# Kernel optimization log

Measured on AMD Instinct MI355X. Metric: run time of the kernel, lower is better.

## Reference

```python
import jax, jax.numpy as jnp
import numpy as np

T, NC, NQ = 16, 32, 32
H, W, C = 128, 128, 1
DW, DR, DZ = 256, 256, 128
LABEL_DIM, Y_DIM = 2, 2
NHEADS = 8
NFEAT = int(DW * np.log(DW))  # performer default nb_features = int(d*ln d) = 1419


def setup_inputs() -> dict:
    key = jax.random.key(0)
    ks = iter(jax.random.split(key, 48))
    def nrm(shape, scale=0.02):
        return jax.random.normal(next(ks), shape, dtype=jnp.float32) * scale
    z = lambda *s: jnp.zeros(s, jnp.float32)
    return {
        'batch_train_images': jax.random.normal(next(ks), (T, NC, C, H, W), jnp.float32),
        'label_train': jax.random.normal(next(ks), (T, NC, LABEL_DIM), jnp.float32),
        'batch_test_images': jax.random.normal(next(ks), (T, NQ, C, H, W), jnp.float32),
        'conv1_w': nrm((32, C, 3, 3), 0.1), 'conv1_b': z(32),
        'conv2_w': nrm((48, 32, 3, 3), 0.05), 'conv2_b': z(48),
        'conv3_w': nrm((64, 48, 3, 3), 0.05), 'conv3_b': z(64),
        'enc_lw': nrm((DW, 4096)), 'enc_lb': z(DW),
        'ty_w': nrm((DW // 4, LABEL_DIM)), 'ty_b': z(DW // 4),
        'er_w1': nrm((DR, DW + DW // 4), 0.05), 'er_b1': z(DR),
        'er_w2': nrm((DR, DR), 0.05), 'er_b2': z(DR),
        'er_w3': nrm((DR, DR), 0.05), 'er_b3': z(DR),
        'wq': nrm((NHEADS, DW, DW), 0.05), 'wq_b': z(NHEADS, DW),
        'wk': nrm((NHEADS, DW, DW), 0.05), 'wk_b': z(NHEADS, DW),
        'wv': nrm((NHEADS, DW, DW), 0.05), 'wv_b': z(NHEADS, DW),
        'wo_w': nrm((DW, NHEADS * DW), 0.02), 'wo_b': z(DW),
        'rz_w': nrm((DZ, DR), 0.05), 'rz_b': z(DZ),
        'd0_w1': nrm((100, DW + DZ), 0.05), 'd0_b1': z(100),
        'd0_w2': nrm((100, 100), 0.05), 'd0_b2': z(100),
        'd0_w3': nrm((Y_DIM, 100), 0.05), 'd0_b3': z(Y_DIM),
        'proj': jax.random.normal(next(ks), (NFEAT, DW), jnp.float32),
    }


def _conv(x, w, b, stride):
    y = jax.lax.conv_general_dilated(x, w, (stride, stride), [(1, 1), (1, 1)],
                                     dimension_numbers=('NCHW', 'OIHW', 'NCHW'))
    return y + b[None, :, None, None]


def _maxpool2(x):
    return jax.lax.reduce_window(x, -jnp.inf, jax.lax.max, (1, 1, 2, 2), (1, 1, 2, 2), 'VALID')


def _encode(x, c1w, c1b, c2w, c2b, c3w, c3b, lw, lb):
    # BBBEncoder (mean weights): 128->64->32->pool16->8, 64ch, flatten 4096 -> DW
    x = jax.nn.relu(_conv(x, c1w, c1b, 2))
    x = jax.nn.relu(_conv(x, c2w, c2b, 2))
    x = _maxpool2(x)
    x = jax.nn.relu(_conv(x, c3w, c3b, 2))
    x = x.reshape(x.shape[0], -1)  # [B, 4096], NCHW order matches torch view
    return x @ lw.T + lb


def _softmax_kernel(x, proj, is_query):
    # performer softmax-kernel random features
    dn = x.shape[-1] ** -0.25
    ratio = proj.shape[0] ** -0.5
    xn = x * dn
    xd = jnp.einsum('bhnd,fd->bhnf', xn, proj)
    diag = 0.5 * jnp.sum(xn * xn, axis=-1, keepdims=True)
    if is_query:
        m = jnp.max(xd, axis=-1, keepdims=True)
    else:
        m = jnp.max(xd, axis=(-1, -2), keepdims=True)
    return ratio * (jnp.exp(xd - diag - jax.lax.stop_gradient(m)) + 1e-4)


def _forward(batch_train_images, label_train, batch_test_images,
             conv1_w, conv1_b, conv2_w, conv2_b, conv3_w, conv3_b, enc_lw, enc_lb,
             ty_w, ty_b, er_w1, er_b1, er_w2, er_b2, er_w3, er_b3,
             wq, wq_b, wk, wk_b, wv, wv_b, wo_w, wo_b, rz_w, rz_b,
             d0_w1, d0_b1, d0_w2, d0_b2, d0_w3, d0_b3, proj):
    enc = lambda im: _encode(im, conv1_w, conv1_b, conv2_w, conv2_b, conv3_w, conv3_b, enc_lw, enc_lb)
    x_qry = enc(batch_test_images.reshape(-1, C, H, W)).reshape(T, NQ, DW)
    x_ctx = enc(batch_train_images.reshape(-1, C, H, W)).reshape(T, NC, DW)
    ly = label_train @ ty_w.T + ty_b
    x = jnp.concatenate([x_ctx, ly], axis=2)  # [T, NC, DW + DW//4]
    h = jax.nn.relu(x @ er_w1.T + er_b1)
    h = jax.nn.relu(h @ er_w2.T + er_b2)
    rs = h @ er_w3.T + er_b3  # [T, NC, DR]
    # per-head projections (batched over the 8 heads)
    k_all = jnp.einsum('bnd,hed->bhne', x_ctx, wk) + wk_b[None, :, None, :]
    v_all = jnp.einsum('bnd,hed->bhne', rs, wv) + wv_b[None, :, None, :]
    q_all = jnp.einsum('bnd,hed->bhne', x_qry, wq) + wq_b[None, :, None, :]
    qp = _softmax_kernel(q_all, proj, True)   # [T, H, NQ, F]
    kp = _softmax_kernel(k_all, proj, False)  # [T, H, NC, F]
    d_inv = 1.0 / jnp.einsum('bhnf,bhf->bhn', qp, kp.sum(axis=2))
    ctx_mat = jnp.einsum('bhnf,bhne->bhfe', kp, v_all)
    outs = jnp.einsum('bhnf,bhfe->bhne', qp, ctx_mat) * d_inv[..., None]
    outs = outs.transpose(0, 2, 3, 1).reshape(T, NQ, -1)  # permute(0,2,3,1).view
    rep = outs @ wo_w.T + wo_b
    zz = rep @ rz_w.T + rz_b  # [T, NQ, DZ]
    xz = jnp.concatenate([x_qry, zz], axis=-1)
    h = jax.nn.relu(xz @ d0_w1.T + d0_b1)
    h = jax.nn.relu(h @ d0_w2.T + d0_b2)
    return jnp.tanh(h @ d0_w3.T + d0_b3)  # pr_y_mu [T, NQ, Y_DIM]


def reference(batch_train_images, label_train, batch_test_images,
              conv1_w, conv1_b, conv2_w, conv2_b, conv3_w, conv3_b, enc_lw, enc_lb,
              ty_w, ty_b, er_w1, er_b1, er_w2, er_b2, er_w3, er_b3,
              wq, wq_b, wk, wk_b, wv, wv_b, wo_w, wo_b, rz_w, rz_b,
              d0_w1, d0_b1, d0_w2, d0_b2, d0_w3, d0_b3, proj):
    pr_y_mu = _forward(batch_train_images, label_train, batch_test_images,
                       conv1_w, conv1_b, conv2_w, conv2_b, conv3_w, conv3_b, enc_lw, enc_lb,
                       ty_w, ty_b, er_w1, er_b1, er_w2, er_b2, er_w3, er_b3,
                       wq, wq_b, wk, wk_b, wv, wv_b, wo_w, wo_b, rz_w, rz_b,
                       d0_w1, d0_b1, d0_w2, d0_b2, d0_w3, d0_b3, proj)
    kl = jnp.float32(0.0)  # deterministic (mean-weight) BBB encoder -> KL constant
    return (pr_y_mu, kl)
```

## Files before the change

kernel.cpp:

```cpp
#include <hip/hip_runtime.h>
#include <math.h>

#define F_FEAT 1419
static constexpr float DN    = 0.25f;

typedef short short8 __attribute__((ext_vector_type(8)));
typedef float f32x4  __attribute__((ext_vector_type(4)));

static constexpr long OFF_XDQ  = 0;
static constexpr long OFF_XDK  = 5812224;
static constexpr long U_WQH = 0;
static constexpr long U_WQL = 524288;
static constexpr long U_WKH = 1048576;
static constexpr long U_WKL = 1572864;
static constexpr long U_WVH = 2097152;
static constexpr long U_WVL = 2621440;
static constexpr long OFF_ENCT = 4000000;
static constexpr long OFF_REPT = 6200000;
static constexpr long OFF_PA   = 11624448;
static constexpr long U_PH  = 23248896;
static constexpr long U_PL  = 23625728;
static constexpr long U_XCH = 24002560;
static constexpr long U_XCL = 24264704;
static constexpr long U_RSH = 24526848;
static constexpr long U_RSL = 24657920;
static constexpr long U_C3H = 25165824;
static constexpr long U_C3L = 29360128;
static constexpr long U_WOH = 25165824;
static constexpr long U_WOL = 25690112;
static constexpr long BASE     = 16777216;
static constexpr long OFF_XCTX = BASE + 0;
static constexpr long OFF_XQRY = BASE + 131072;
static constexpr long OFF_XCAT = BASE + 262144;
static constexpr long OFF_H1   = BASE + 425984;
static constexpr long OFF_H2   = BASE + 557056;
static constexpr long OFF_RS   = BASE + 688128;
static constexpr long U_QH  = (BASE + 819200) * 2;
static constexpr long U_QL  = U_QH + 1048576;
static constexpr long U_KH  = (BASE + 1867776) * 2;
static constexpr long U_KL  = U_KH + 1048576;
static constexpr long OFF_VA   = BASE + 2916352;
static constexpr long OFF_AW1  = BASE + 3964928;
static constexpr long U_ELH = (BASE + 3977344) * 2;
static constexpr long U_ELL = U_ELH + 1048576;
static constexpr long U_REPH = U_ELH;
static constexpr long U_REPL = U_ELL;
static constexpr long OFF_REP  = BASE + 5025920;
static constexpr long OFF_XZ   = BASE + 5156992;
static constexpr long OFF_DH1  = BASE + 5353600;
static constexpr long OFF_DH2  = BASE + 5404800;
static constexpr long OFF_MD   = BASE + 5456000;
static constexpr long OFF_AW   = 22233216;
static constexpr long OFF_AW3  = 22240128;

__device__ inline unsigned short f2bf(float f) {
    unsigned int x = __float_as_uint(f);
    unsigned int r = x + 0x7fffu + ((x >> 16) & 1u);
    return (unsigned short)(r >> 16);
}
__device__ inline float bf2f(unsigned short h) {
    return __uint_as_float((unsigned int)h << 16);
}
__device__ inline unsigned int cvtpk(float a, float b) {
    unsigned int r;
    asm("v_cvt_pk_bf16_f32 %0, %1, %2" : "=v"(r) : "v"(a), "v"(b));
    return r;
}
__device__ inline unsigned encf(float f) {
    unsigned u = __float_as_uint(f);
    return (u & 0x80000000u) ? ~u : (u | 0x80000000u);
}
__device__ inline float decf(unsigned u) {
    return __uint_as_float((u & 0x80000000u) ? (u & 0x7fffffffu) : ~u);
}

static constexpr int NA1 = 13824;
static constexpr int NA2 = NA1 + 1024;
static constexpr int NA3 = NA2 + 73728;
static constexpr int NA4 = NA3 + 1048576;

__global__ void k_wprepA(const float* __restrict__ w2, const float* __restrict__ w1,
                         const float* __restrict__ w3, const float* __restrict__ elw,
                         unsigned short* __restrict__ Aw, unsigned short* __restrict__ Aw1,
                         unsigned short* __restrict__ Aw3,
                         unsigned short* __restrict__ ELh, unsigned short* __restrict__ ELl)
{
    int i = blockIdx.x * 256 + threadIdx.x;
    if (i < NA1) {
        int ic  = i & 31;
        int m16 = (i >> 5) & 15;
        int emt = i >> 9;
        int mt  = emt % 3, e = emt / 3;
        Aw[i] = f2bf(w2[((mt * 16 + m16) * 32 + ic) * 9 + e]);
    } else if (i < NA2) {
        int j = i - NA1;
        int k = j & 31, m = (j >> 5) & 15, mt = j >> 9;
        Aw1[j] = (k < 9) ? f2bf(w1[(mt * 16 + m) * 9 + k]) : (unsigned short)0;
    } else if (i < NA3) {
        int j = i - NA2;
        int k  = j & 63;
        int m  = (j >> 6) & 15;
        int hl = (j >> 10) & 1;
        int mt = (j >> 11) & 3;
        int e  = j >> 13;
        unsigned short v = 0;
        if (k < 48) {
            float w = w3[((mt * 16 + m) * 48 + k) * 9 + e];
            unsigned short hi = f2bf(w);
            v = hl == 0 ? hi : f2bf(w - bf2f(hi));
        }
        Aw3[j] = v;
    } else if (i < NA4) {
        int j = i - NA3;
        float v = elw[j];
        unsigned short h = f2bf(v);
        ELh[j] = h; ELl[j] = f2bf(v - bf2f(h));
    }
}

static constexpr int NB1 = 376832;
static constexpr int NB2 = NB1 + 1572864;

__global__ void k_wprepB(const float* __restrict__ proj,
                         const float* __restrict__ wq, const float* __restrict__ wk,
                         const float* __restrict__ wv,
                         unsigned short* __restrict__ Ph, unsigned short* __restrict__ Pl,
                         unsigned short* __restrict__ Wqkv)
{
    int i = blockIdx.x * 256 + threadIdx.x;
    if (i < NB1) {
        float v = (i < 363264) ? proj[i] : 0.f;
        unsigned short h = f2bf(v);
        Ph[i] = h; Pl[i] = f2bf(v - bf2f(h));
    } else if (i < NB2) {
        int j = i - NB1;
        int y = j / 524288, jj = j % 524288;
        const float* s = (y == 0) ? wq : (y == 1) ? wk : wv;
        float v = s[jj];
        unsigned short h = f2bf(v);
        Wqkv[(long)y * 1048576 + jj] = h;
        Wqkv[(long)y * 1048576 + 524288 + jj] = f2bf(v - bf2f(h));
    }
}

#define TP 136
__launch_bounds__(256)
__global__ void k_conv12m(const float* __restrict__ train, const float* __restrict__ test,
                          const float* __restrict__ b1,
                          const unsigned short* __restrict__ Aw,
                          const unsigned short* __restrict__ Aw1,
                          const float* __restrict__ b2,
                          unsigned short* __restrict__ pool_out)
{
    const int g   = blockIdx.x;
    const int img = blockIdx.y;
    const float* in = (img < 512) ? (train + (long)img * 16384)
                                  : (test  + (long)(img - 512) * 16384);

    __shared__ unsigned short ring[9 * 66 * 40];
    __shared__ unsigned short tile[19 * TP];

    const int t = threadIdx.x;

    for (int i = t; i < 9 * 40; i += 256) {
        int sl = i / 40, icp = i % 40;
        ring[(sl * 66 + 0) * 40 + icp] = 0;
    }
    if (g == 0)
        for (int i = t; i < 66 * 40; i += 256) ring[i] = 0;
    if (t < 19) *(unsigned int*)&tile[t * TP + 2] = 0u;

    {
        const float4 z4 = make_float4(0.f, 0.f, 0.f, 0.f);
        for (int u = t; u < 19 * 32; u += 256) {
            int row = u >> 5, k = u & 31;
            int r2 = 16 * g - 3 + row;
            float4 v = (r2 >= 0) ? *(const float4*)(in + r2 * 128 + k * 4) : z4;
            uint2 d;
            d.x = cvtpk(v.x, v.y);
            d.y = cvtpk(v.z, v.w);
            *(uint2*)&tile[row * TP + 4 + k * 4] = d;
        }
    }
    __syncthreads();

    const int w    = t >> 6;
    const int lane = t & 63;
    const int cn   = lane & 15;
    const int quad = lane >> 4;

    short8 a1f0 = *(const short8*)&Aw1[(0 * 16 + cn) * 32 + quad * 8];
    short8 a1f1 = *(const short8*)&Aw1[(16 + cn) * 32 + quad * 8];
    float4 bsa = *(const float4*)&b1[quad * 4];
    float4 bsb = *(const float4*)&b1[16 + quad * 4];

    const int px2 = w * 16 + cn;
    const int tb  = 2 * px2 + 2;
    auto do_slice = [&](int sl) {
        const int rb = 2 * sl * TP + tb;
        uint4 pk = make_uint4(0u, 0u, 0u, 0u);
        if (quad == 0) {
            unsigned int w00 = *(const unsigned int*)&tile[rb];
            unsigned int w10 = *(const unsigned int*)&tile[rb + 2];
            unsigned int w01 = *(const unsigned int*)&tile[rb + TP];
            unsigned int w11 = *(const unsigned int*)&tile[rb + TP + 2];
            unsigned int w02 = *(const unsigned int*)&tile[rb + 2 * TP];
            unsigned int w12 = *(const unsigned int*)&tile[rb + 2 * TP + 2];
            pk.x = (w00 >> 16) | (w10 << 16);
            pk.y = (w10 >> 16) | (w01 & 0xffff0000u);
            pk.z = w11;
            pk.w = (w02 >> 16) | (w12 << 16);
        } else if (quad == 1) {
            pk.x = (*(const unsigned int*)&tile[rb + 2 * TP + 2]) >> 16;
        }
        short8 bfr = *(const short8*)&pk;
        f32x4 z = (f32x4){0.f, 0.f, 0.f, 0.f};
        f32x4 c0 = __builtin_amdgcn_mfma_f32_16x16x32_bf16(a1f0, bfr, z, 0, 0, 0);
        f32x4 c1 = __builtin_amdgcn_mfma_f32_16x16x32_bf16(a1f1, bfr, z, 0, 0, 0);
        uint2 u0, u1;
        u0.x = cvtpk(fmaxf(c0[0] + bsa.x, 0.f), fmaxf(c0[1] + bsa.y, 0.f));
        u0.y = cvtpk(fmaxf(c0[2] + bsa.z, 0.f), fmaxf(c0[3] + bsa.w, 0.f));
        u1.x = cvtpk(fmaxf(c1[0] + bsb.x, 0.f), fmaxf(c1[1] + bsb.y, 0.f));
        u1.y = cvtpk(fmaxf(c1[2] + bsb.z, 0.f), fmaxf(c1[3] + bsb.w, 0.f));
        *(uint2*)&ring[(sl * 66 + px2 + 1) * 40 + quad * 4]      = u0;
        *(uint2*)&ring[(sl * 66 + px2 + 1) * 40 + 16 + quad * 4] = u1;
    };
    if (g > 0) do_slice(0);
    #pragma unroll
    for (int sl = 1; sl < 9; sl++) do_slice(sl);

    short8 ca0 = *(const short8*)&Aw[((0 * 3 + 0) * 16 + cn) * 32 + quad * 8];
    short8 ca1 = *(const short8*)&Aw[((0 * 3 + 1) * 16 + cn) * 32 + quad * 8];
    short8 ca2 = *(const short8*)&Aw[((0 * 3 + 2) * 16 + cn) * 32 + quad * 8];
    __syncthreads();

    const int pr = w >> 1, xh = w & 1;
    f32x4 acc[3][2];
    #pragma unroll
    for (int mt = 0; mt < 3; mt++) {
        acc[mt][0] = (f32x4){0.f, 0.f, 0.f, 0.f};
        acc[mt][1] = (f32x4){0.f, 0.f, 0.f, 0.f};
    }

    #pragma unroll
    for (int e = 0; e < 9; e++) {
        int dy = e / 3, dx = e - 3 * dy;
        int c  = 2 * (xh * 16 + cn) + dx;
        int s0 = 4 * pr + dy;
        short8 b0  = *(const short8*)&ring[(s0 * 66 + c) * 40 + quad * 8];
        short8 b1f = *(const short8*)&ring[((s0 + 2) * 66 + c) * 40 + quad * 8];
        short8 na0, na1, na2;
        if (e < 8) {
            na0 = *(const short8*)&Aw[(((e + 1) * 3 + 0) * 16 + cn) * 32 + quad * 8];
            na1 = *(const short8*)&Aw[(((e + 1) * 3 + 1) * 16 + cn) * 32 + quad * 8];
            na2 = *(const short8*)&Aw[(((e + 1) * 3 + 2) * 16 + cn) * 32 + quad * 8];
        }
        acc[0][0] = __builtin_amdgcn_mfma_f32_16x16x32_bf16(ca0, b0,  acc[0][0], 0, 0, 0);
        acc[1][0] = __builtin_amdgcn_mfma_f32_16x16x32_bf16(ca1, b0,  acc[1][0], 0, 0, 0);
        acc[2][0] = __builtin_amdgcn_mfma_f32_16x16x32_bf16(ca2, b0,  acc[2][0], 0, 0, 0);
        acc[0][1] = __builtin_amdgcn_mfma_f32_16x16x32_bf16(ca0, b1f, acc[0][1], 0, 0, 0);
        acc[1][1] = __builtin_amdgcn_mfma_f32_16x16x32_bf16(ca1, b1f, acc[1][1], 0, 0, 0);
        acc[2][1] = __builtin_amdgcn_mfma_f32_16x16x32_bf16(ca2, b1f, acc[2][1], 0, 0, 0);
        if (e < 8) { ca0 = na0; ca1 = na1; ca2 = na2; }
    }

    {
        const int prow = 2 * g + pr;
        const int ppx  = xh * 8 + (cn >> 1);
        unsigned short* pb = pool_out + ((long)img * 256 + prow * 16 + ppx) * 96
                           + ((cn & 1) ? 48 : 0);
        #pragma unroll
        for (int mt = 0; mt < 3; mt++) {
            float4 bv = *(const float4*)&b2[mt * 16 + quad * 4];
            float m0, m1, m2, m3;
            {
                float v;
                v = fmaxf(fmaxf(acc[mt][0][0] + bv.x, acc[mt][1][0] + bv.x), 0.f);
                m0 = fmaxf(v, __shfl_xor(v, 1));
                v = fmaxf(fmaxf(acc[mt][0][1] + bv.y, acc[mt][1][1] + bv.y), 0.f);
                m1 = fmaxf(v, __shfl_xor(v, 1));
                v = fmaxf(fmaxf(acc[mt][0][2] + bv.z, acc[mt][1][2] + bv.z), 0.f);
                m2 = fmaxf(v, __shfl_xor(v, 1));
                v = fmaxf(fmaxf(acc[mt][0][3] + bv.w, acc[mt][1][3] + bv.w), 0.f);
                m3 = fmaxf(v, __shfl_xor(v, 1));
            }
            uint2 hv;
            hv.x = cvtpk(m0, m1);
            hv.y = cvtpk(m2, m3);
            uint2 sv = hv;
            if (cn & 1) {
                float d0 = m0 - bf2f((unsigned short)(hv.x & 0xffffu));
                float d1 = m1 - bf2f((unsigned short)(hv.x >> 16));
                float d2 = m2 - bf2f((unsigned short)(hv.y & 0xffffu));
                float d3 = m3 - bf2f((unsigned short)(hv.y >> 16));
                sv.x = cvtpk(d0, d1);
                sv.y = cvtpk(d2, d3);
            }
            *(uint2*)&pb[mt * 16 + quad * 4] = sv;
        }
    }
}

#define C3PITCH 104
__launch_bounds__(512)
__global__ void k_conv3m(const unsigned short* __restrict__ pool,
                         const unsigned short* __restrict__ Aw3,
                         const float* __restrict__ b3,
                         unsigned short* __restrict__ C3h, unsigned short* __restrict__ C3l)
{
    const int img = blockIdx.x;
    __shared__ unsigned short s_in[30120];
    const int t = threadIdx.x;

    uint4* s4 = (uint4*)s_in;
    const uint4 zz = make_uint4(0, 0, 0, 0);
    for (int i = t; i < 3765; i += 512) s4[i] = zz;
    __syncthreads();
    {
        int p = t >> 1, half = t & 1;
        const uint4* src = (const uint4*)(pool + ((long)img * 256 + p) * 96 + half * 48);
        int r = p >> 4, c = p & 15;
        uint4* dst = (uint4*)(s_in + ((r + 1) * 17 + (c + 1)) * C3PITCH + half * 48);
        #pragma unroll
        for (int j = 0; j < 6; j++) dst[j] = src[j];
    }
    __syncthreads();

    const int w = t >> 6, lane = t & 63;
    const int n = lane & 15, quad = lane >> 4;
    const int mt = w >> 1, ntb = (w & 1) * 2;

    f32x4 acc[2];
    acc[0] = (f32x4){0.f, 0.f, 0.f, 0.f};
    acc[1] = (f32x4){0.f, 0.f, 0.f, 0.f};

    for (int e = 0; e < 9; e++) {
        int dy = e / 3, dx = e - 3 * dy;
        const unsigned short* A0 = Aw3 + (long)(((e * 4 + mt) * 2 + 0) * 16 + n) * 64 + quad * 8;
        const unsigned short* A1 = Aw3 + (long)(((e * 4 + mt) * 2 + 1) * 16 + n) * 64 + quad * 8;
        short8 ah0 = *(const short8*)(A0);
        short8 ah1 = *(const short8*)(A0 + 32);
        short8 al0 = *(const short8*)(A1);
        short8 al1 = *(const short8*)(A1 + 32);
        #pragma unroll
        for (int j = 0; j < 2; j++) {
            int p = (ntb + j) * 16 + n;
            int y = p >> 3, x = p & 7;
            const unsigned short* Bp = s_in + ((2 * y + dy) * 17 + (2 * x + dx)) * C3PITCH + quad * 8;
            short8 bh0 = *(const short8*)(Bp);
            short8 bh1 = *(const short8*)(Bp + 32);
            short8 bl0 = *(const short8*)(Bp + 48);
            short8 bl1 = *(const short8*)(Bp + 48 + 32);
            acc[j] = __builtin_amdgcn_mfma_f32_16x16x32_bf16(ah0, bh0, acc[j], 0, 0, 0);
            acc[j] = __builtin_amdgcn_mfma_f32_16x16x32_bf16(ah1, bh1, acc[j], 0, 0, 0);
            acc[j] = __builtin_amdgcn_mfma_f32_16x16x32_bf16(ah0, bl0, acc[j], 0, 0, 0);
            acc[j] = __builtin_amdgcn_mfma_f32_16x16x32_bf16(ah1, bl1, acc[j], 0, 0, 0);
            acc[j] = __builtin_amdgcn_mfma_f32_16x16x32_bf16(al0, bh0, acc[j], 0, 0, 0);
            acc[j] = __builtin_amdgcn_mfma_f32_16x16x32_bf16(al1, bh1, acc[j], 0, 0, 0);
        }
    }

    unsigned short* oh = C3h + (long)img * 4096;
    unsigned short* ol = C3l + (long)img * 4096;
    #pragma unroll
    for (int reg = 0; reg < 4; reg++) {
        int oc = mt * 16 + quad * 4 + reg;
        float bias = b3[oc];
        #pragma unroll
        for (int j = 0; j < 2; j++) {
            int p = (ntb + j) * 16 + n;
            float v = fmaxf(acc[j][reg] + bias, 0.f);
            unsigned short h = f2bf(v);
            oh[oc * 64 + p] = h;
            ol[oc * 64 + p] = f2bf(v - bf2f(h));
        }
    }
}

template<int OUTMODE>
__launch_bounds__(256)
__global__ void mgemm(const unsigned short* __restrict__ Xh0, const unsigned short* __restrict__ Xl0,
                      const unsigned short* __restrict__ Wph, const unsigned short* __restrict__ Wpl,
                      const float* __restrict__ Bb, float* __restrict__ Yf,
                      unsigned short* __restrict__ Yh, unsigned short* __restrict__ Yl,
                      int M, int N, int K, int ldY, float scale,
                      long sX, long sW, long sB, long sY, int kChunk,
                      unsigned* __restrict__ mqe, unsigned* __restrict__ mke)
{
    const int z = blockIdx.z;
    const unsigned short* Xh = Xh0 + (OUTMODE == 3 ? 0 : (long)z * sX);
    const unsigned short* Xl = Xl0 + (OUTMODE == 3 ? 0 : (long)z * sX);
    const unsigned short* Wh = Wph + (OUTMODE == 3 ? 0 : (long)z * sW);
    const unsigned short* Wl = Wpl + (OUTMODE == 3 ? 0 : (long)z * sW);
    const float* B = Bb ? (Bb + (OUTMODE == 3 ? 0 : (long)z * sB)) : nullptr;
    int k0 = 0, k1 = K;
    if (OUTMODE == 3) { k0 = z * kChunk; k1 = min(K, k0 + kChunk); }

    __shared__ unsigned short sAh[64 * 40], sAl[64 * 40], sBh[64 * 40], sBl[64 * 40];

    const int t = threadIdx.x;
    const int m0 = blockIdx.y * 64, n0 = blockIdx.x * 64;
    const int r = t >> 2, kq = (t & 3) * 8;

    const int w = t >> 6, lane = t & 63;
    const int wm = (w & 1) * 32, wn = (w >> 1) * 32;
    const int cn = lane & 15, quad = lane >> 4;

    f32x4 acc[2][2];
    acc[0][0] = acc[0][1] = acc[1][0] = acc[1][1] = (f32x4){0.f, 0.f, 0.f, 0.f};

    for (int kb = k0; kb < k1; kb += 32) {
        *(uint4*)&sAh[r * 40 + kq] = *(const uint4*)&Xh[(long)(m0 + r) * K + kb + kq];
        *(uint4*)&sAl[r * 40 + kq] = *(const uint4*)&Xl[(long)(m0 + r) * K + kb + kq];
        *(uint4*)&sBh[r * 40 + kq] = *(const uint4*)&Wh[(long)(n0 + r) * K + kb + kq];
        *(uint4*)&sBl[r * 40 + kq] = *(const uint4*)&Wl[(long)(n0 + r) * K + kb + kq];
        __syncthreads();
        short8 axh[2], axl[2], bxh[2], bxl[2];
        #pragma unroll
        for (int i = 0; i < 2; i++) {
            axh[i] = *(const short8*)&sAh[(wm + i * 16 + cn) * 40 + quad * 8];
            axl[i] = *(const short8*)&sAl[(wm + i * 16 + cn) * 40 + quad * 8];
            bxh[i] = *(const short8*)&sBh[(wn + i * 16 + cn) * 40 + quad * 8];
            bxl[i] = *(const short8*)&sBl[(wn + i * 16 + cn) * 40 + quad * 8];
        }
        #pragma unroll
        for (int i = 0; i < 2; i++)
            #pragma unroll
            for (int j = 0; j < 2; j++) {
                acc[i][j] = __builtin_amdgcn_mfma_f32_16x16x32_bf16(axh[i], bxh[j], acc[i][j], 0, 0, 0);
                acc[i][j] = __builtin_amdgcn_mfma_f32_16x16x32_bf16(axh[i], bxl[j], acc[i][j], 0, 0, 0);
                acc[i][j] = __builtin_amdgcn_mfma_f32_16x16x32_bf16(axl[i], bxh[j], acc[i][j], 0, 0, 0);
            }
        __syncthreads();
    }

    float gmax = -3e38f;
    #pragma unroll
    for (int i = 0; i < 2; i++) {
        #pragma unroll
        for (int reg = 0; reg < 4; reg++) {
            int row = m0 + wm + i * 16 + quad * 4 + reg;
            float rmax = -3e38f;
            #pragma unroll
            for (int j = 0; j < 2; j++) {
                int col = n0 + wn + j * 16 + cn;
                if (col >= N) continue;
                float v = acc[i][j][reg] * scale;
                if (OUTMODE == 3) {
                    (Yf + (long)z * sY)[(long)row * ldY + col] = v;
                } else if (OUTMODE == 0 || OUTMODE == 5) {
                    if (B) v += B[col];
                    (Yf + (long)z * sY)[(long)row * ldY + col] = v;
                    if (OUTMODE == 5) rmax = fmaxf(rmax, v);
                } else {
                    if (B) v += B[col];
                    unsigned short h = f2bf(v);
                    (Yh + (long)z * sY)[(long)row * ldY + col] = h;
                    (Yl + (long)z * sY)[(long)row * ldY + col] = f2bf(v - bf2f(h));
                }
            }
            if (OUTMODE == 5) {
                if (z == 0) {
                    rmax = fmaxf(rmax, __shfl_xor(rmax, 1));
                    rmax = fmaxf(rmax, __shfl_xor(rmax, 2));
                    rmax = fmaxf(rmax, __shfl_xor(rmax, 4));
                    rmax = fmaxf(rmax, __shfl_xor(rmax, 8));
                    if (cn == 0) atomicMax(&mqe[row], encf(rmax));
                } else {
                    gmax = fmaxf(gmax, rmax);
                }
            }
        }
    }
    if (OUTMODE == 5 && z == 1) {
        for (int d = 1; d < 64; d <<= 1) gmax = fmaxf(gmax, __shfl_xor(gmax, d));
        if (lane == 0) atomicMax(&mke[(m0 + wm) >> 5], encf(gmax));
    }
}

__launch_bounds__(256)
__global__ void k_qkv(const unsigned short* __restrict__ XCh, const unsigned short* __restrict__ XCl,
                      const unsigned short* __restrict__ RSh, const unsigned short* __restrict__ RSl,
                      const unsigned short* __restrict__ Wqkv,
                      const float* __restrict__ wqb, const float* __restrict__ wkb,
                      const float* __restrict__ wvb,
                      unsigned short* __restrict__ Qh, unsigned short* __restrict__ Ql,
                      unsigned short* __restrict__ Kh, unsigned short* __restrict__ Kl,
                      float* __restrict__ v_all, float* __restrict__ dq, float* __restrict__ dk)
{
    const int z = blockIdx.z, y = z >> 3, zh = z & 7;
    const unsigned short* Xh = (y == 0) ? XCh + 512 * 256 : (y == 1) ? XCh : RSh;
    const unsigned short* Xl = (y == 0) ? XCl + 512 * 256 : (y == 1) ? XCl : RSl;
    const unsigned short* Wh = Wqkv + (long)y * 1048576 + (long)zh * 65536;
    const unsigned short* Wl = Wh + 524288;
    const float* B = ((y == 0) ? wqb : (y == 1) ? wkb : wvb) + zh * 256;

    __shared__ unsigned short sAh[64 * 40], sAl[64 * 40], sBh[64 * 40], sBl[64 * 40];

    const int t = threadIdx.x;
    const int m0 = blockIdx.y * 64, n0 = blockIdx.x * 64;
    const int r = t >> 2, kq = (t & 3) * 8;
    const int w = t >> 6, lane = t & 63;
    const int wm = (w & 1) * 32, wn = (w >> 1) * 32;
    const int cn = lane & 15, quad = lane >> 4;

    f32x4 acc[2][2];
    acc[0][0] = acc[0][1] = acc[1][0] = acc[1][1] = (f32x4){0.f, 0.f, 0.f, 0.f};

    for (int kb = 0; kb < 256; kb += 32) {
        *(uint4*)&sAh[r * 40 + kq] = *(const uint4*)&Xh[(long)(m0 + r) * 256 + kb + kq];
        *(uint4*)&sAl[r * 40 + kq] = *(const uint4*)&Xl[(long)(m0 + r) * 256 + kb + kq];
        *(uint4*)&sBh[r * 40 + kq] = *(const uint4*)&Wh[(long)(n0 + r) * 256 + kb + kq];
        *(uint4*)&sBl[r * 40 + kq] = *(const uint4*)&Wl[(long)(n0 + r) * 256 + kb + kq];
        __syncthreads();
        short8 axh[2], axl[2], bxh[2], bxl[2];
        #pragma unroll
        for (int i = 0; i < 2; i++) {
            axh[i] = *(const short8*)&sAh[(wm + i * 16 + cn) * 40 + quad * 8];
            axl[i] = *(const short8*)&sAl[(wm + i * 16 + cn) * 40 + quad * 8];
            bxh[i] = *(const short8*)&sBh[(wn + i * 16 + cn) * 40 + quad * 8];
            bxl[i] = *(const short8*)&sBl[(wn + i * 16 + cn) * 40 + quad * 8];
        }
        #pragma unroll
        for (int i = 0; i < 2; i++)
            #pragma unroll
            for (int j = 0; j < 2; j++) {
                acc[i][j] = __builtin_amdgcn_mfma_f32_16x16x32_bf16(axh[i], bxh[j], acc[i][j], 0, 0, 0);
                acc[i][j] = __builtin_amdgcn_mfma_f32_16x16x32_bf16(axh[i], bxl[j], acc[i][j], 0, 0, 0);
                acc[i][j] = __builtin_amdgcn_mfma_f32_16x16x32_bf16(axl[i], bxh[j], acc[i][j], 0, 0, 0);
            }
        __syncthreads();
    }

    unsigned short* Yh = ((y == 0) ? Qh : Kh) + (long)zh * 131072;
    unsigned short* Yl = ((y == 0) ? Ql : Kl) + (long)zh * 131072;
    float* Yf = v_all + (long)zh * 131072;
    float* dacc = ((y == 0) ? dq : dk) + zh * 512;

    #pragma unroll
    for (int i = 0; i < 2; i++) {
        #pragma unroll
        for (int reg = 0; reg < 4; reg++) {
            int row = m0 + wm + i * 16 + quad * 4 + reg;
            float s = 0.f;
            #pragma unroll
            for (int j = 0; j < 2; j++) {
                int col = n0 + wn + j * 16 + cn;
                float v = acc[i][j][reg] + B[col];
                if (y == 2) {
                    Yf[(long)row * 256 + col] = v;
                } else {
                    unsigned short h = f2bf(v);
                    Yh[(long)row * 256 + col] = h;
                    Yl[(long)row * 256 + col] = f2bf(v - bf2f(h));
                    s += v * v;
                }
            }
            if (y < 2) {
                s += __shfl_xor(s, 1); s += __shfl_xor(s, 2);
                s += __shfl_xor(s, 4); s += __shfl_xor(s, 8);
                if (cn == 0) atomicAdd(&dacc[row], s * (1.f / 32.f));
            }
        }
    }
}

__global__ void k_red_enc(const float* __restrict__ tmp, const float* __restrict__ elb,
                          float* __restrict__ x_ctx, unsigned short* __restrict__ XCh,
                          unsigned short* __restrict__ XCl, float* __restrict__ xcat,
                          const float* __restrict__ label, const float* __restrict__ tyw,
                          const float* __restrict__ tyb,
                          const float* __restrict__ wow, unsigned short* __restrict__ WOh,
                          unsigned short* __restrict__ WOl, unsigned* __restrict__ md)
{
    int b = blockIdx.x;
    int tt = threadIdx.x;
    if (b < 1024) {
        int i = b * 256 + tt;
        int r = i >> 8, c = i & 255;
        float v = elb[c];
        #pragma unroll
        for (int z = 0; z < 8; z++) v += tmp[(long)z * 262144 + i];
        x_ctx[i] = v;
        unsigned short h = f2bf(v);
        XCh[i] = h; XCl[i] = f2bf(v - bf2f(h));
        if (r < 512) xcat[r * 320 + c] = v;
    } else if (b < 1152) {
        int i = (b - 1024) * 256 + tt;
        int r = i >> 6, e = i & 63;
        xcat[r * 320 + 256 + e] = tyb[e] + label[r * 2] * tyw[e * 2] + label[r * 2 + 1] * tyw[e * 2 + 1];
    } else if (b < 3200) {
        int i = (b - 1152) * 256 + tt;
        float v = wow[i];
        unsigned short h = f2bf(v);
        WOh[i] = h; WOl[i] = f2bf(v - bf2f(h));
    } else {
        int i = (b - 3200) * 256 + tt;
        if (i < 12416) md[i] = 0u;
    }
}

__global__ void k_red_rep(const float* __restrict__ tmp, const float* __restrict__ wob,
                          float* __restrict__ rep,
                          const float* __restrict__ xq, float* __restrict__ xz)
{
    int b = blockIdx.x;
    int tt = threadIdx.x;
    if (b < 512) {
        int i = b * 256 + tt;
        int c = i & 255;
        float v = wob[c];
        #pragma unroll
        for (int z = 0; z < 8; z++) v += tmp[(long)z * 131072 + i];
        rep[i] = v;
    } else {
        int i = (b - 512) * 256 + tt;
        int r = i >> 8, c = i & 255;
        xz[r * 384 + c] = xq[i];
    }
}

template<int BM, int BN, int BK, int ACT, bool FIN, bool WP>
__launch_bounds__(256)
__global__ void gemm_k(const float* __restrict__ X, const float* __restrict__ W,
                       const float* __restrict__ B, float* __restrict__ Y,
                       int M, int N, int K, int ldY,
                       unsigned short* __restrict__ Ph2, unsigned short* __restrict__ Pl2)
{
    __shared__ float As[BK][BM + 4];
    __shared__ float Bs[BK][BN + 4];
    const int t = threadIdx.x;
    const int tx = t & 15, ty = t >> 4;
    const int m0 = blockIdx.y * BM, n0 = blockIdx.x * BN;
    float acc[2][2] = {{0.f, 0.f}, {0.f, 0.f}};

    for (int kb = 0; kb < K; kb += BK) {
        for (int i = t; i < BM * BK; i += 256) {
            int rr = i / BK, c = i % BK;
            int mm = m0 + rr, kk = kb + c;
            As[c][rr] = (mm < M && kk < K) ? X[(long)mm * K + kk] : 0.f;
        }
        for (int i = t; i < BN * BK; i += 256) {
            int rr = i / BK, c = i % BK;
            int nn = n0 + rr, kk = kb + c;
            Bs[c][rr] = (nn < N && kk < K) ? W[(long)nn * K + kk] : 0.f;
        }
        __syncthreads();
        #pragma unroll
        for (int kk = 0; kk < BK; kk++) {
            float2 a2 = *(const float2*)&As[kk][ty * 2];
            float2 b2 = *(const float2*)&Bs[kk][tx * 2];
            acc[0][0] += a2.x * b2.x; acc[0][1] += a2.x * b2.y;
            acc[1][0] += a2.y * b2.x; acc[1][1] += a2.y * b2.y;
        }
        __syncthreads();
    }

    #pragma unroll
    for (int i = 0; i < 2; i++) {
        int mm = m0 + ty * 2 + i;
        if (mm >= M) continue;
        #pragma unroll
        for (int j = 0; j < 2; j++) {
            int nn = n0 + tx * 2 + j;
            if (nn >= N) continue;
            float v = acc[i][j] + (B ? B[nn] : 0.f);
            if (ACT == 1) v = fmaxf(v, 0.f);
            if (ACT == 2) v = tanhf(v);
            Y[(long)mm * ldY + nn] = v;
            if (WP) {
                unsigned short h = f2bf(v);
                Ph2[(long)mm * ldY + nn] = h;
                Pl2[(long)mm * ldY + nn] = f2bf(v - bf2f(h));
            }
        }
    }
    if (FIN && t == 0 && blockIdx.x == 0 && blockIdx.y == 0) Y[1024] = 0.f;
}

#define NSPLIT 4
#define FCH 355
__launch_bounds__(256)
__global__ void k_attn1(const float* __restrict__ qp, const float* __restrict__ kp,
                        const float* __restrict__ dq, const unsigned* __restrict__ mqe,
                        const float* __restrict__ dk, const unsigned* __restrict__ mke,
                        float* __restrict__ pA)
{
    const int s  = blockIdx.x;
    const int kb = blockIdx.y;
    const long row0 = (long)kb * 32;
    const int f0 = s * FCH;
    const int f1 = min(F_FEAT, f0 + FCH);

    __shared__ float s_q[32 * 65];
    __shared__ float s_k[32 * 65];
    __shared__ float s_cq[32], s_ck[32];

    const int t = threadIdx.x;
    const int n = t >> 3;
    const int mq_ = (t & 7) * 4;

    if (t < 32) {
        s_cq[t] = dq[row0 + t] + decf(mqe[row0 + t]);
        s_ck[t] = dk[row0 + t] + decf(mke[kb]);
    }
    __syncthreads();

    float acc[4] = {0.f, 0.f, 0.f, 0.f};
    for (int fc = f0; fc < f1; fc += 64) {
        for (int i = t; i < 2048; i += 256) {
            int rr = i >> 6, ff = i & 63;
            int fg = fc + ff;
            float qv = 0.f, kv = 0.f;
            if (fg < f1) {
                qv = __expf(qp[(row0 + rr) * F_FEAT + fg] - s_cq[rr]) + 1e-4f;
                kv = __expf(kp[(row0 + rr) * F_FEAT + fg] - s_ck[rr]) + 1e-4f;
            }
            s_q[rr * 65 + ff] = qv;
            s_k[rr * 65 + ff] = kv;
        }
        __syncthreads();
        #pragma unroll 8
        for (int ff = 0; ff < 64; ff++) {
            float a = s_q[n * 65 + ff];
            #pragma unroll
            for (int j = 0; j < 4; j++) acc[j] += a * s_k[(mq_ + j) * 65 + ff];
        }
        __syncthreads();
    }

    float* dst = pA + ((long)kb * NSPLIT + s) * 1024;
    #pragma unroll
    for (int j = 0; j < 4; j++) dst[n * 32 + mq_ + j] = acc[j];
}

__launch_bounds__(256)
__global__ void k_attn2(const float* __restrict__ pA, const float* __restrict__ va,
                        unsigned short* __restrict__ REPh, unsigned short* __restrict__ REPl)
{
    const int ec = blockIdx.x;
    const int kb = blockIdx.y;
    const int h = kb >> 4, tt = kb & 15;
    const long row0 = (long)kb * 32;

    __shared__ float s_A[32][33];
    __shared__ float s_di[32];
    __shared__ float s_v[32 * 64];

    const int t = threadIdx.x;

    {
        const float* base = pA + (long)kb * NSPLIT * 1024 + t * 4;
        float4 v0 = *(const float4*)(base);
        float4 v1 = *(const float4*)(base + 1024);
        float4 v2 = *(const float4*)(base + 2048);
        float4 v3 = *(const float4*)(base + 3072);
        int r = t >> 3, c = (t & 7) * 4;
        s_A[r][c]     = v0.x + v1.x + v2.x + v3.x;
        s_A[r][c + 1] = v0.y + v1.y + v2.y + v3.y;
        s_A[r][c + 2] = v0.z + v1.z + v2.z + v3.z;
        s_A[r][c + 3] = v0.w + v1.w + v2.w + v3.w;
    }
    for (int i = t; i < 2048; i += 256) {
        int m = i >> 6, e = i & 63;
        s_v[m * 64 + e] = va[row0 * 256 + m * 256 + ec * 64 + e];
    }
    __syncthreads();
    if (t < 32) {
        float s = 0.f;
        #pragma unroll
        for (int m = 0; m < 32; m++) s += s_A[t][m];
        s_di[t] = 1.f / s;
    }
    __syncthreads();

    const int n = t >> 3, e0 = t & 7;
    float out[8];
    #pragma unroll
    for (int j = 0; j < 8; j++) out[j] = 0.f;
    for (int m = 0; m < 32; m++) {
        float a = s_A[n][m];
        #pragma unroll
        for (int j = 0; j < 8; j++) out[j] += a * s_v[m * 64 + e0 + 8 * j];
    }
    float di = s_di[n];
    unsigned short* dsth = REPh + ((long)tt * 32 + n) * 2048;
    unsigned short* dstl = REPl + ((long)tt * 32 + n) * 2048;
    #pragma unroll
    for (int j = 0; j < 8; j++) {
        int e = ec * 64 + e0 + 8 * j;
        float val = out[j] * di;
        unsigned short hh = f2bf(val);
        dsth[e * 8 + h] = hh;
        dstl[e * 8 + h] = f2bf(val - bf2f(hh));
    }
}

extern "C" void kernel_launch(void* const* d_in, const int* in_sizes, int n_in,
                              void* d_out, int out_size, void* d_ws, size_t ws_size,
                              hipStream_t stream)
{
    const float* train  = (const float*)d_in[0];
    const float* label  = (const float*)d_in[1];
    const float* test   = (const float*)d_in[2];
    const float* c1w = (const float*)d_in[3];  const float* c1b = (const float*)d_in[4];
    const float* c2w = (const float*)d_in[5];  const float* c2b = (const float*)d_in[6];
    const float* c3w = (const float*)d_in[7];  const float* c3b = (const float*)d_in[8];
    const float* elw = (const float*)d_in[9];  const float* elb = (const float*)d_in[10];
    const float* tyw = (const float*)d_in[11]; const float* tyb = (const float*)d_in[12];
    const float* ew1 = (const float*)d_in[13]; const float* eb1 = (const float*)d_in[14];
    const float* ew2 = (const float*)d_in[15]; const float* eb2 = (const float*)d_in[16];
    const float* ew3 = (const float*)d_in[17]; const float* eb3 = (const float*)d_in[18];
    const float* wq  = (const float*)d_in[19]; const float* wqb = (const float*)d_in[20];
    const float* wk  = (const float*)d_in[21]; const float* wkb = (const float*)d_in[22];
    const float* wv  = (const float*)d_in[23]; const float* wvb = (const float*)d_in[24];
    const float* wow = (const float*)d_in[25]; const float* wob = (const float*)d_in[26];
    const float* rzw = (const float*)d_in[27]; const float* rzb = (const float*)d_in[28];
    const float* dw1 = (const float*)d_in[29]; const float* db1 = (const float*)d_in[30];
    const float* dw2 = (const float*)d_in[31]; const float* db2 = (const float*)d_in[32];
    const float* dw3 = (const float*)d_in[33]; const float* db3 = (const float*)d_in[34];
    const float* proj= (const float*)d_in[35];

    float* wsf = (float*)d_ws;
    unsigned short* usw = (unsigned short*)d_ws;
    float* out = (float*)d_out;

    unsigned short* A_pool = usw;
    float* x_ctx  = wsf + OFF_XCTX;
    float* x_qry  = wsf + OFF_XQRY;
    float* xcat   = wsf + OFF_XCAT;
    float* h1     = wsf + OFF_H1;
    float* h2     = wsf + OFF_H2;
    float* rs     = wsf + OFF_RS;
    float* v_all  = wsf + OFF_VA;
    float* rep    = wsf + OFF_REP;
    float* xz     = wsf + OFF_XZ;
    float* dh1    = wsf + OFF_DH1;
    float* dh2    = wsf + OFF_DH2;
    float* xd_q   = wsf + OFF_XDQ;
    float* xd_k   = wsf + OFF_XDK;
    float* enc_t  = wsf + OFF_ENCT;
    float* rep_t  = wsf + OFF_REPT;
    float* pA     = wsf + OFF_PA;
    float* dqv    = wsf + OFF_MD;
    unsigned* mqe = (unsigned*)(wsf + OFF_MD + 4096);
    float* dkv    = wsf + OFF_MD + 8192;
    unsigned* mke = (unsigned*)(wsf + OFF_MD + 12288);
    unsigned* mdw = (unsigned*)(wsf + OFF_MD);
    unsigned short* Aw  = (unsigned short*)(wsf + OFF_AW);
    unsigned short* Aw3 = (unsigned short*)(wsf + OFF_AW3);
    unsigned short* Aw1 = (unsigned short*)(wsf + OFF_AW1);

    unsigned short* Wqkv = usw + U_WQH;
    unsigned short* Ph  = usw + U_PH;  unsigned short* Pl  = usw + U_PL;
    unsigned short* XCh = usw + U_XCH; unsigned short* XCl = usw + U_XCL;
    unsigned short* RSh = usw + U_RSH; unsigned short* RSl = usw + U_RSL;
    unsigned short* C3h = usw + U_C3H; unsigned short* C3l = usw + U_C3L;
    unsigned short* Qh  = usw + U_QH;  unsigned short* Ql  = usw + U_QL;
    unsigned short* Kh  = usw + U_KH;  unsigned short* Kl  = usw + U_KL;
    unsigned short* ELh = usw + U_ELH; unsigned short* ELl = usw + U_ELL;
    unsigned short* WOh = usw + U_WOH; unsigned short* WOl = usw + U_WOL;
    unsigned short* REPh= usw + U_REPH;unsigned short* REPl= usw + U_REPL;

    k_wprepA<<<4442, 256, 0, stream>>>(c2w, c1w, c3w, elw, Aw, Aw1, Aw3, ELh, ELl);

    k_conv12m<<<dim3(8, 1024), 256, 0, stream>>>(train, test, c1b, Aw, Aw1, c2b, A_pool);
    k_conv3m<<<1024, 512, 0, stream>>>(A_pool, Aw3, c3b, C3h, C3l);

    k_wprepB<<<7616, 256, 0, stream>>>(proj, wq, wk, wv, Ph, Pl, Wqkv);

    mgemm<3><<<dim3(4, 16, 8), 256, 0, stream>>>(
        C3h, C3l, ELh, ELl, nullptr, enc_t, nullptr, nullptr,
        1024, 256, 4096, 256, 1.f, 0, 0, 0, 262144, 512, nullptr, nullptr);
    k_red_enc<<<3249, 256, 0, stream>>>(enc_t, elb, x_ctx, XCh, XCl, xcat,
                                        label, tyw, tyb, wow, WOh, WOl, mdw);

    gemm_k<32,32,32,1,false,false><<<dim3(8, 16), 256, 0, stream>>>(xcat, ew1, eb1, h1, 512, 256, 320, 256, nullptr, nullptr);
    gemm_k<32,32,32,1,false,false><<<dim3(8, 16), 256, 0, stream>>>(h1, ew2, eb2, h2, 512, 256, 256, 256, nullptr, nullptr);
    gemm_k<32,32,32,0,false,true ><<<dim3(8, 16), 256, 0, stream>>>(h2, ew3, eb3, rs, 512, 256, 256, 256, RSh, RSl);

    k_qkv<<<dim3(4, 8, 24), 256, 0, stream>>>(XCh, XCl, RSh, RSl, Wqkv,
                                              wqb, wkb, wvb, Qh, Ql, Kh, Kl,
                                              v_all, dqv, dkv);

    mgemm<5><<<dim3(23, 64, 2), 256, 0, stream>>>(
        Qh, Ql, Ph, Pl, nullptr, xd_q, nullptr, nullptr,
        4096, F_FEAT, 256, F_FEAT, DN, 2097152, 0, 0, 5812224, 0, mqe, mke);

    k_attn1<<<dim3(NSPLIT, 128), 256, 0, stream>>>(xd_q, xd_k, dqv, mqe, dkv, mke, pA);
    k_attn2<<<dim3(4, 128), 256, 0, stream>>>(pA, v_all, REPh, REPl);

    mgemm<3><<<dim3(4, 8, 8), 256, 0, stream>>>(
        REPh, REPl, WOh, WOl, nullptr, rep_t, nullptr, nullptr,
        512, 256, 2048, 256, 1.f, 0, 0, 0, 131072, 256, nullptr, nullptr);
    k_red_rep<<<1024, 256, 0, stream>>>(rep_t, wob, rep, x_qry, xz);

    gemm_k<32,32,32,0,false,false><<<dim3(4, 16), 256, 0, stream>>>(rep, rzw, rzb, xz + 256, 512, 128, 256, 384, nullptr, nullptr);

    gemm_k<32,32,32,1,false,false><<<dim3(4, 16), 256, 0, stream>>>(xz, dw1, db1, dh1, 512, 100, 384, 100, nullptr, nullptr);
    gemm_k<32,32,32,1,false,false><<<dim3(4, 16), 256, 0, stream>>>(dh1, dw2, db2, dh2, 512, 100, 100, 100, nullptr, nullptr);
    gemm_k<32,32,32,2,true ,false><<<dim3(1, 16), 256, 0, stream>>>(dh2, dw3, db3, out, 512, 2, 100, 2, nullptr, nullptr);
}
```

Measured before the change: 650.1 us.

## Double conv12 block threads, split conv2 rows per wave, pool via LDS

The fused conv1+conv2+pool kernel now runs with 512 threads instead of 256. The conv1 slice work is spread over 8 waves, and each wave computes one conv2 output row instead of two, using half the accumulators. The 2x2 max-pool and hi/lo bf16 split move from lane shuffles to a pass through an LDS scratch buffer that reuses the ring memory, with extra barriers. The aim is more waves in flight and lower register pressure, at the cost of extra LDS traffic, added syncs and dropping the A-fragment prefetch.

```diff
diff --git a/kernel.cpp b/kernel.cpp
--- a/kernel.cpp
+++ b/kernel.cpp
@@ -144,7 +144,7 @@
 }
 
 #define TP 136
-__launch_bounds__(256)
+__launch_bounds__(512)
 __global__ void k_conv12m(const float* __restrict__ train, const float* __restrict__ test,
                           const float* __restrict__ b1,
                           const unsigned short* __restrict__ Aw,
@@ -159,20 +159,21 @@
 
     __shared__ unsigned short ring[9 * 66 * 40];
     __shared__ unsigned short tile[19 * TP];
+    float* scratch = (float*)ring;
 
     const int t = threadIdx.x;
 
-    for (int i = t; i < 9 * 40; i += 256) {
-        int sl = i / 40, icp = i % 40;
+    if (t < 9 * 40) {
+        int sl = t / 40, icp = t % 40;
         ring[(sl * 66 + 0) * 40 + icp] = 0;
     }
     if (g == 0)
-        for (int i = t; i < 66 * 40; i += 256) ring[i] = 0;
-    if (t < 19) *(unsigned int*)&tile[t * TP + 2] = 0u;
+        for (int i = t; i < 66 * 40; i += 512) ring[i] = 0;
+    if (t >= 64 && t < 83) *(unsigned int*)&tile[(t - 64) * TP + 2] = 0u;
 
     {
         const float4 z4 = make_float4(0.f, 0.f, 0.f, 0.f);
-        for (int u = t; u < 19 * 32; u += 256) {
+        for (int u = t; u < 19 * 32; u += 512) {
             int row = u >> 5, k = u & 31;
             int r2 = 16 * g - 3 + row;
             float4 v = (r2 >= 0) ? *(const float4*)(in + r2 * 128 + k * 4) : z4;
@@ -194,10 +195,8 @@
     float4 bsa = *(const float4*)&b1[quad * 4];
     float4 bsb = *(const float4*)&b1[16 + quad * 4];
 
-    const int px2 = w * 16 + cn;
-    const int tb  = 2 * px2 + 2;
-    auto do_slice = [&](int sl) {
-        const int rb = 2 * sl * TP + tb;
+    auto do_slice = [&](int sl, int px2) {
+        const int rb = 2 * sl * TP + 2 * px2 + 2;
         uint4 pk = make_uint4(0u, 0u, 0u, 0u);
         if (quad == 0) {
             unsigned int w00 = *(const unsigned int*)&tile[rb];
@@ -225,79 +224,51 @@
         *(uint2*)&ring[(sl * 66 + px2 + 1) * 40 + quad * 4]      = u0;
         *(uint2*)&ring[(sl * 66 + px2 + 1) * 40 + 16 + quad * 4] = u1;
     };
-    if (g > 0) do_slice(0);
-    #pragma unroll
-    for (int sl = 1; sl < 9; sl++) do_slice(sl);
-
-    short8 ca0 = *(const short8*)&Aw[((0 * 3 + 0) * 16 + cn) * 32 + quad * 8];
-    short8 ca1 = *(const short8*)&Aw[((0 * 3 + 1) * 16 + cn) * 32 + quad * 8];
-    short8 ca2 = *(const short8*)&Aw[((0 * 3 + 2) * 16 + cn) * 32 + quad * 8];
+    for (int u = w; u < 36; u += 8) {
+        int sl = u >> 2, pg = u & 3;
+        if (!(g == 0 && sl == 0)) do_slice(sl, pg * 16 + cn);
+    }
     __syncthreads();
 
-    const int pr = w >> 1, xh = w & 1;
-    f32x4 acc[3][2];
-    #pragma unroll
-    for (int mt = 0; mt < 3; mt++) {
-        acc[mt][0] = (f32x4){0.f, 0.f, 0.f, 0.f};
-        acc[mt][1] = (f32x4){0.f, 0.f, 0.f, 0.f};
-    }
+    const int cr = w >> 1, xh = w & 1;
+    f32x4 acc[3];
+    acc[0] = acc[1] = acc[2] = (f32x4){0.f, 0.f, 0.f, 0.f};
 
     #pragma unroll
     for (int e = 0; e < 9; e++) {
         int dy = e / 3, dx = e - 3 * dy;
+        short8 a0 = *(const short8*)&Aw[((e * 3 + 0) * 16 + cn) * 32 + quad * 8];
+        short8 a1 = *(const short8*)&Aw[((e * 3 + 1) * 16 + cn) * 32 + quad * 8];
+        short8 a2 = *(const short8*)&Aw[((e * 3 + 2) * 16 + cn) * 32 + quad * 8];
         int c  = 2 * (xh * 16 + cn) + dx;
-        int s0 = 4 * pr + dy;
-        short8 b0  = *(const short8*)&ring[(s0 * 66 + c) * 40 + quad * 8];
-        short8 b1f = *(const short8*)&ring[((s0 + 2) * 66 + c) * 40 + quad * 8];
-        short8 na0, na1, na2;
-        if (e < 8) {
-            na0 = *(const short8*)&Aw[(((e + 1) * 3 + 0) * 16 + cn) * 32 + quad * 8];
-            na1 = *(const short8*)&Aw[(((e + 1) * 3 + 1) * 16 + cn) * 32 + quad * 8];
-            na2 = *(const short8*)&Aw[(((e + 1) * 3 + 2) * 16 + cn) * 32 + quad * 8];
-        }
-        acc[0][0] = __builtin_amdgcn_mfma_f32_16x16x32_bf16(ca0, b0,  acc[0][0], 0, 0, 0);
-        acc[1][0] = __builtin_amdgcn_mfma_f32_16x16x32_bf16(ca1, b0,  acc[1][0], 0, 0, 0);
-        acc[2][0] = __builtin_amdgcn_mfma_f32_16x16x32_bf16(ca2, b0,  acc[2][0], 0, 0, 0);
-        acc[0][1] = __builtin_amdgcn_mfma_f32_16x16x32_bf16(ca0, b1f, acc[0][1], 0, 0, 0);
-        acc[1][1] = __builtin_amdgcn_mfma_f32_16x16x32_bf16(ca1, b1f, acc[1][1], 0, 0, 0);
-        acc[2][1] = __builtin_amdgcn_mfma_f32_16x16x32_bf16(ca2, b1f, acc[2][1], 0, 0, 0);
-        if (e < 8) { ca0 = na0; ca1 = na1; ca2 = na2; }
-    }
-
-    {
-        const int prow = 2 * g + pr;
-        const int ppx  = xh * 8 + (cn >> 1);
-        unsigned short* pb = pool_out + ((long)img * 256 + prow * 16 + ppx) * 96
-                           + ((cn & 1) ? 48 : 0);
-        #pragma unroll
-        for (int mt = 0; mt < 3; mt++) {
-            float4 bv = *(const float4*)&b2[mt * 16 + quad * 4];
-            float m0, m1, m2, m3;
-            {
-                float v;
-                v = fmaxf(fmaxf(acc[mt][0][0] + bv.x, acc[mt][1][0] + bv.x), 0.f);
-                m0 = fmaxf(v, __shfl_xor(v, 1));
-                v = fmaxf(fmaxf(acc[mt][0][1] + bv.y, acc[mt][1][1] + bv.y), 0.f);
-                m1 = fmaxf(v, __shfl_xor(v, 1));
-                v = fmaxf(fmaxf(acc[mt][0][2] + bv.z, acc[mt][1][2] + bv.z), 0.f);
-                m2 = fmaxf(v, __shfl_xor(v, 1));
-                v = fmaxf(fmaxf(acc[mt][0][3] + bv.w, acc[mt][1][3] + bv.w), 0.f);
-                m3 = fmaxf(v, __shfl_xor(v, 1));
-            }
-            uint2 hv;
-            hv.x = cvtpk(m0, m1);
-            hv.y = cvtpk(m2, m3);
-            uint2 sv = hv;
-            if (cn & 1) {
-                float d0 = m0 - bf2f((unsigned short)(hv.x & 0xffffu));
-                float d1 = m1 - bf2f((unsigned short)(hv.x >> 16));
-                float d2 = m2 - bf2f((unsigned short)(hv.y & 0xffffu));
-                float d3 = m3 - bf2f((unsigned short)(hv.y >> 16));
-                sv.x = cvtpk(d0, d1);
-                sv.y = cvtpk(d2, d3);
-            }
-            *(uint2*)&pb[mt * 16 + quad * 4] = sv;
-        }
+        short8 bfr = *(const short8*)&ring[((2 * cr + dy) * 66 + c) * 40 + quad * 8];
+        acc[0] = __builtin_amdgcn_mfma_f32_16x16x32_bf16(a0, bfr, acc[0], 0, 0, 0);
+        acc[1] = __builtin_amdgcn_mfma_f32_16x16x32_bf16(a1, bfr, acc[1], 0, 0, 0);
+        acc[2] = __builtin_amdgcn_mfma_f32_16x16x32_bf16(a2, bfr, acc[2], 0, 0, 0);
+    }
+    __syncthreads();
+
+    #pragma unroll
+    for (int mt = 0; mt < 3; mt++) {
+        float4 bv = *(const float4*)&b2[mt * 16 + quad * 4];
+        int x = xh * 16 + cn;
+        float* sr = &scratch[(cr * 32 + x) * 52 + mt * 16 + quad * 4];
+        sr[0] = fmaxf(acc[mt][0] + bv.x, 0.f);
+        sr[1] = fmaxf(acc[mt][1] + bv.y, 0.f);
+        sr[2] = fmaxf(acc[mt][2] + bv.z, 0.f);
+        sr[3] = fmaxf(acc[mt][3] + bv.w, 0.f);
+    }
+    __syncthreads();
+
+    for (int i = t; i < 1536; i += 512) {
+        int oc = i % 48; int pp = i / 48; int px = pp & 15, pr = pp >> 4;
+        const float* b0 = &scratch[((2 * pr) * 32 + 2 * px) * 52 + oc];
+        float m = fmaxf(fmaxf(b0[0], b0[52]), fmaxf(b0[32 * 52], b0[33 * 52]));
+        unsigned short hi = f2bf(m);
+        unsigned short lo = f2bf(m - bf2f(hi));
+        long base = ((long)img * 256 + (2 * g + pr) * 16 + px) * 96;
+        pool_out[base + oc] = hi;
+        pool_out[base + 48 + oc] = lo;
     }
 }
 
@@ -864,7 +835,7 @@
 
     k_wprepA<<<4442, 256, 0, stream>>>(c2w, c1w, c3w, elw, Aw, Aw1, Aw3, ELh, ELl);
 
-    k_conv12m<<<dim3(8, 1024), 256, 0, stream>>>(train, test, c1b, Aw, Aw1, c2b, A_pool);
+    k_conv12m<<<dim3(8, 1024), 512, 0, stream>>>(train, test, c1b, Aw, Aw1, c2b, A_pool);
     k_conv3m<<<1024, 512, 0, stream>>>(A_pool, Aw3, c3b, C3h, C3l);
 
     k_wprepB<<<7616, 256, 0, stream>>>(proj, wq, wk, wv, Ph, Pl, Wqkv);
```

New measurement: 689.1 us. +6.0%, slower.
